# Performance work log

Measured on AMD Instinct MI355X. Metric: run time of the kernel, lower is better.

The kernel has to match this reference:

```python
import jax, jax.numpy as jnp
import numpy as np

N_AUTHORS = 50000
N_PAPERS = 100000
N_NODES = N_AUTHORS + N_PAPERS
N_EDGES = 1200000
EMB_DIM = 64
NUM_LAYERS = 3


def setup_inputs() -> dict:
    key = jax.random.key(0)
    k1, k2, k3, k4, k5 = jax.random.split(key, 5)
    author_embedding = jax.random.normal(k1, (N_AUTHORS, EMB_DIM), dtype=jnp.float32)
    paper_embedding = jax.random.normal(k2, (N_PAPERS, EMB_DIM), dtype=jnp.float32)
    adj_rows = jax.random.randint(k3, (N_EDGES,), 0, N_NODES, dtype=jnp.int32)
    adj_cols = jax.random.randint(k4, (N_EDGES,), 0, N_NODES, dtype=jnp.int32)
    # symmetric-normalized adjacency values are small positive floats
    adj_vals = jax.random.uniform(k5, (N_EDGES,), dtype=jnp.float32) * 0.1
    return {
        "author_embedding": author_embedding,
        "paper_embedding": paper_embedding,
        "adj_rows": adj_rows,
        "adj_cols": adj_cols,
        "adj_vals": adj_vals,
    }


def _spmm(adj_rows, adj_cols, adj_vals, x):
    # sparse [N,N] @ dense [N,d] via gather + segment_sum
    msgs = adj_vals[:, None] * x[adj_cols]  # [E, d]
    return jax.ops.segment_sum(msgs, adj_rows, num_segments=N_NODES)


def reference(author_embedding, paper_embedding, adj_rows, adj_cols, adj_vals):
    ego = jnp.concatenate([author_embedding, paper_embedding], axis=0)  # [N, d]
    acc = ego
    x = ego
    for _ in range(NUM_LAYERS):
        x = _spmm(adj_rows, adj_cols, adj_vals, x)
        acc = acc + x
    out = acc / jnp.float32(NUM_LAYERS + 1)  # mean over layer outputs
    out_author = out[:N_AUTHORS]
    out_paper = out[N_AUTHORS:]
    return ego, out_author, out_paper
```

## Files before the change

### kernel.cpp

```cpp
#include <hip/hip_runtime.h>

#define N_AUTHORS 50000
#define N_PAPERS  100000
#define N_NODES   150000
#define N_EDGES   1200000
#define EMB       64

#define BSHIFT 10
#define K_B    ((N_NODES + 1023) >> 10)
#define CHUNK  4096
#define NBLK_A ((N_EDGES + CHUNK - 1) / CHUNK)
#define NSC    (K_B * NBLK_A)
#define NBS1   ((NSC + 1023) / 1024)

__device__ __forceinline__ float bf2f(ushort u) {
    return __uint_as_float(((unsigned)u) << 16);
}
__device__ __forceinline__ ushort f2bf(float f) {
    unsigned u = __float_as_uint(f);
    return (ushort)((u + 0x7fffu + ((u >> 16) & 1u)) >> 16);
}

__global__ void lgcn_init(const float* __restrict__ a,
                          const float* __restrict__ p,
                          float* __restrict__ ego_out,
                          ushort* __restrict__ x0) {
    size_t i = (size_t)blockIdx.x * blockDim.x + threadIdx.x;
    const size_t n4  = (size_t)N_NODES  * EMB / 4;
    const size_t au4 = (size_t)N_AUTHORS * EMB / 4;
    if (i >= n4) return;
    float4 v = (i < au4) ? ((const float4*)a)[i] : ((const float4*)p)[i - au4];
    ((float4*)ego_out)[i] = v;
    ushort4 b;
    b.x = f2bf(v.x); b.y = f2bf(v.y); b.z = f2bf(v.z); b.w = f2bf(v.w);
    ((ushort4*)x0)[i] = b;
}

__global__ void lgcn_a0_hist(const int* __restrict__ rows,
                             unsigned* __restrict__ counts) {
    __shared__ unsigned h[K_B];
    int t = threadIdx.x;
    for (int i = t; i < K_B; i += blockDim.x) h[i] = 0;
    __syncthreads();
    int base = blockIdx.x * CHUNK;
    int end  = base + CHUNK; if (end > N_EDGES) end = N_EDGES;
    for (int e = base + t; e < end; e += blockDim.x)
        atomicAdd(&h[rows[e] >> BSHIFT], 1u);
    __syncthreads();
    for (int i = t; i < K_B; i += blockDim.x)
        counts[(size_t)i * NBLK_A + blockIdx.x] = h[i];
}

__global__ void lgcn_scan_l1(const unsigned* __restrict__ counts,
                             unsigned* __restrict__ scanned,
                             unsigned* __restrict__ btot) {
    __shared__ unsigned s[1024];
    int t = threadIdx.x;
    int i = blockIdx.x * 1024 + t;
    unsigned v = (i < NSC) ? counts[i] : 0u;
    s[t] = v;
    __syncthreads();
    for (int d = 1; d < 1024; d <<= 1) {
        unsigned u = (t >= d) ? s[t - d] : 0u;
        __syncthreads();
        s[t] += u;
        __syncthreads();
    }
    if (i < NSC) scanned[i] = s[t] - v;
    if (t == 1023) btot[blockIdx.x] = s[1023];
}

__global__ void lgcn_scan_l2(const unsigned* __restrict__ btot,
                             unsigned* __restrict__ btot_ex) {
    __shared__ unsigned s[64];
    int t = threadIdx.x;
    unsigned v = (t < NBS1) ? btot[t] : 0u;
    s[t] = v;
    __syncthreads();
    for (int d = 1; d < 64; d <<= 1) {
        unsigned u = (t >= d) ? s[t - d] : 0u;
        __syncthreads();
        s[t] += u;
        __syncthreads();
    }
    btot_ex[t] = s[t] - v;
}

__device__ __forceinline__ unsigned scan_at(const unsigned* scanned,
                                            const unsigned* btot_ex, unsigned idx) {
    return scanned[idx] + btot_ex[idx >> 10];
}

__global__ void lgcn_a1_bin(const int* __restrict__ rows,
                            const int* __restrict__ cols,
                            const float* __restrict__ vals,
                            const unsigned* __restrict__ scanned,
                            const unsigned* __restrict__ btot_ex,
                            float2* __restrict__ stage) {
    __shared__ unsigned cur[K_B];
    int t = threadIdx.x;
    for (int i = t; i < K_B; i += blockDim.x)
        cur[i] = scan_at(scanned, btot_ex, (unsigned)i * NBLK_A + blockIdx.x);
    __syncthreads();
    int base = blockIdx.x * CHUNK;
    int end  = base + CHUNK; if (end > N_EDGES) end = N_EDGES;
    for (int e = base + t; e < end; e += blockDim.x) {
        int r = rows[e];
        unsigned pos = atomicAdd(&cur[r >> BSHIFT], 1u);
        unsigned packed = ((unsigned)(r & 1023) << 18) | (unsigned)cols[e];
        stage[pos] = make_float2(__uint_as_float(packed), vals[e]);
    }
}

__global__ void lgcn_place(const unsigned* __restrict__ scanned,
                           const unsigned* __restrict__ btot_ex,
                           const float2* __restrict__ stage,
                           float2* __restrict__ se,
                           unsigned* __restrict__ row_start) {
    __shared__ unsigned cur[1 << BSHIFT];
    __shared__ unsigned tsum[256];
    int b  = blockIdx.x;
    int rb = b << BSHIFT;
    int nrows = N_NODES - rb; if (nrows > (1 << BSHIFT)) nrows = 1 << BSHIFT;
    int t = threadIdx.x;

    unsigned base  = scan_at(scanned, btot_ex, (unsigned)b * NBLK_A);
    unsigned span1 = (b + 1 < K_B)
                   ? scan_at(scanned, btot_ex, (unsigned)(b + 1) * NBLK_A)
                   : N_EDGES;

    for (int i = t; i < (1 << BSHIFT); i += 256) cur[i] = 0;
    __syncthreads();
    for (unsigned p = base + t; p < span1; p += 256)
        atomicAdd(&cur[__float_as_uint(stage[p].x) >> 18], 1u);
    __syncthreads();

    unsigned c[4], s = 0;
#pragma unroll
    for (int k = 0; k < 4; ++k) { c[k] = cur[t * 4 + k]; s += c[k]; }
    tsum[t] = s;
    __syncthreads();
    for (int d = 1; d < 256; d <<= 1) {
        unsigned u = (t >= d) ? tsum[t - d] : 0u;
        __syncthreads();
        tsum[t] += u;
        __syncthreads();
    }
    unsigned run = base + (tsum[t] - s);
    __syncthreads();
#pragma unroll
    for (int k = 0; k < 4; ++k) {
        int i = t * 4 + k;
        cur[i] = run;
        if (i < nrows) row_start[rb + i] = run;
        run += c[k];
    }
    if (b == K_B - 1 && t == 0) row_start[N_NODES] = N_EDGES;
    __syncthreads();

    for (unsigned p = base + t; p < span1; p += 256) {
        float2 v = stage[p];
        unsigned u = __float_as_uint(v.x);
        unsigned pos = atomicAdd(&cur[u >> 18], 1u);
        se[pos] = make_float2(__int_as_float((int)(u & 0x3FFFFu)), v.y);
    }
}

template <int FINAL>
__global__ void lgcn_spmm(const unsigned* __restrict__ rs,
                          const float2* __restrict__ se,
                          const ushort* __restrict__ x,
                          ushort* __restrict__ y,
                          const float* __restrict__ ego,
                          const ushort* __restrict__ y1,
                          const ushort* __restrict__ y2,
                          float* __restrict__ out) {
    int w    = blockIdx.x * (blockDim.x >> 6) + (threadIdx.x >> 6);
    int lane = threadIdx.x & 63;
    if (w >= N_NODES) return;
    unsigned j   = rs[w];
    unsigned end = rs[w + 1];
    const int g  = lane >> 3;
    const int d8 = (lane & 7) << 3;
    float a0=0.f,a1=0.f,a2=0.f,a3=0.f,a4=0.f,a5=0.f,a6=0.f,a7=0.f;

#define BATCH(JBASE)                                                          \
    {                                                                         \
        unsigned idx = (JBASE) + g;                                           \
        float2 e;                                                             \
        if (idx < end) e = se[idx];                                           \
        else { e.x = __int_as_float(0); e.y = 0.f; }                          \
        const uint4 xv = *(const uint4*)(x + ((size_t)__float_as_int(e.x) << 6) + d8); \
        a0 += e.y * __uint_as_float(xv.x << 16);                              \
        a1 += e.y * __uint_as_float(xv.x & 0xffff0000u);                      \
        a2 += e.y * __uint_as_float(xv.y << 16);                              \
        a3 += e.y * __uint_as_float(xv.y & 0xffff0000u);                      \
        a4 += e.y * __uint_as_float(xv.z << 16);                              \
        a5 += e.y * __uint_as_float(xv.z & 0xffff0000u);                      \
        a6 += e.y * __uint_as_float(xv.w << 16);                              \
        a7 += e.y * __uint_as_float(xv.w & 0xffff0000u);                      \
    }

    if (end - j > 8) {
        BATCH(j) BATCH(j + 8)
        j += 16;
    } else {
        BATCH(j)
        j += 8;
    }
    while (j < end) { BATCH(j) j += 8; }
#undef BATCH

    a0 += __shfl_xor(a0, 8, 64); a0 += __shfl_xor(a0, 16, 64); a0 += __shfl_xor(a0, 32, 64);
    a1 += __shfl_xor(a1, 8, 64); a1 += __shfl_xor(a1, 16, 64); a1 += __shfl_xor(a1, 32, 64);
    a2 += __shfl_xor(a2, 8, 64); a2 += __shfl_xor(a2, 16, 64); a2 += __shfl_xor(a2, 32, 64);
    a3 += __shfl_xor(a3, 8, 64); a3 += __shfl_xor(a3, 16, 64); a3 += __shfl_xor(a3, 32, 64);
    a4 += __shfl_xor(a4, 8, 64); a4 += __shfl_xor(a4, 16, 64); a4 += __shfl_xor(a4, 32, 64);
    a5 += __shfl_xor(a5, 8, 64); a5 += __shfl_xor(a5, 16, 64); a5 += __shfl_xor(a5, 32, 64);
    a6 += __shfl_xor(a6, 8, 64); a6 += __shfl_xor(a6, 16, 64); a6 += __shfl_xor(a6, 32, 64);
    a7 += __shfl_xor(a7, 8, 64); a7 += __shfl_xor(a7, 16, 64); a7 += __shfl_xor(a7, 32, 64);

    if (g == 0) {
        size_t o = ((size_t)w << 6) + d8;
        if (FINAL) {
            float4 e0 = *(const float4*)(ego + o);
            float4 e1 = *(const float4*)(ego + o + 4);
            uint4  u1 = *(const uint4*)(y1 + o);
            uint4  u2 = *(const uint4*)(y2 + o);
            float4 r0, r1;
            r0.x = 0.25f * (e0.x + __uint_as_float(u1.x << 16)        + __uint_as_float(u2.x << 16)        + a0);
            r0.y = 0.25f * (e0.y + __uint_as_float(u1.x & 0xffff0000u)+ __uint_as_float(u2.x & 0xffff0000u)+ a1);
            r0.z = 0.25f * (e0.z + __uint_as_float(u1.y << 16)        + __uint_as_float(u2.y << 16)        + a2);
            r0.w = 0.25f * (e0.w + __uint_as_float(u1.y & 0xffff0000u)+ __uint_as_float(u2.y & 0xffff0000u)+ a3);
            r1.x = 0.25f * (e1.x + __uint_as_float(u1.z << 16)        + __uint_as_float(u2.z << 16)        + a4);
            r1.y = 0.25f * (e1.y + __uint_as_float(u1.z & 0xffff0000u)+ __uint_as_float(u2.z & 0xffff0000u)+ a5);
            r1.z = 0.25f * (e1.z + __uint_as_float(u1.w << 16)        + __uint_as_float(u2.w << 16)        + a6);
            r1.w = 0.25f * (e1.w + __uint_as_float(u1.w & 0xffff0000u)+ __uint_as_float(u2.w & 0xffff0000u)+ a7);
            *(float4*)(out + o)     = r0;
            *(float4*)(out + o + 4) = r1;
        } else {
            uint4 ov;
            ov.x = (unsigned)f2bf(a0) | ((unsigned)f2bf(a1) << 16);
            ov.y = (unsigned)f2bf(a2) | ((unsigned)f2bf(a3) << 16);
            ov.z = (unsigned)f2bf(a4) | ((unsigned)f2bf(a5) << 16);
            ov.w = (unsigned)f2bf(a6) | ((unsigned)f2bf(a7) << 16);
            *(uint4*)(y + o) = ov;
        }
    }
}

extern "C" void kernel_launch(void* const* d_in, const int* in_sizes, int n_in,
                              void* d_out, int out_size, void* d_ws, size_t ws_size,
                              hipStream_t stream) {
    const float* author = (const float*)d_in[0];
    const float* paper  = (const float*)d_in[1];
    const int*   rows   = (const int*)d_in[2];
    const int*   cols   = (const int*)d_in[3];
    const float* vals   = (const float*)d_in[4];

    float* ego_out = (float*)d_out;
    float* acc     = (float*)d_out + (size_t)N_NODES * EMB;

    char* w = (char*)d_ws;
    float2*   se        = (float2*)w;   w += (size_t)N_EDGES * sizeof(float2);
    float2*   stage     = (float2*)w;   w += (size_t)N_EDGES * sizeof(float2);
    ushort*   xbE       = (ushort*)w;   w += (size_t)N_NODES * EMB * sizeof(ushort);
    ushort*   xb1       = (ushort*)w;   w += (size_t)N_NODES * EMB * sizeof(ushort);
    ushort*   xb2       = (ushort*)w;   w += (size_t)N_NODES * EMB * sizeof(ushort);
    unsigned* row_start = (unsigned*)w; w += (size_t)(N_NODES + 1) * 4;
    unsigned* bcounts   = (unsigned*)w; w += (size_t)NSC * 4;
    unsigned* bscanned  = (unsigned*)w; w += (size_t)NSC * 4;
    unsigned* btot      = (unsigned*)w; w += 64 * 4;
    unsigned* btot_ex   = (unsigned*)w; w += 64 * 4;

    const int BLK = 256;
    const int g_vec  = (int)(((size_t)N_NODES * EMB / 4 + BLK - 1) / BLK);
    const int g_spmm = (N_NODES + 3) / 4;

    lgcn_init<<<g_vec, BLK, 0, stream>>>(author, paper, ego_out, xbE);

    lgcn_a0_hist<<<NBLK_A, BLK, 0, stream>>>(rows, bcounts);
    lgcn_scan_l1<<<NBS1, 1024, 0, stream>>>(bcounts, bscanned, btot);
    lgcn_scan_l2<<<1, 64, 0, stream>>>(btot, btot_ex);

    lgcn_a1_bin<<<NBLK_A, BLK, 0, stream>>>(rows, cols, vals, bscanned, btot_ex, stage);
    lgcn_place<<<K_B, BLK, 0, stream>>>(bscanned, btot_ex, stage, se, row_start);

    lgcn_spmm<0><<<g_spmm, BLK, 0, stream>>>(row_start, se, xbE, xb1, nullptr, nullptr, nullptr, nullptr);
    lgcn_spmm<0><<<g_spmm, BLK, 0, stream>>>(row_start, se, xb1, xb2, nullptr, nullptr, nullptr, nullptr);
    lgcn_spmm<1><<<g_spmm, BLK, 0, stream>>>(row_start, se, xb2, nullptr, ego_out, xb1, xb2, acc);
}
```

Measured before the change: 212.9 us.

## Process two rows per wavefront in SpMM and read bf16 ego in final layer

Each 64-lane wavefront now handles two adjacent CSR rows, issuing their first gather batches back to back so two independent loads are in flight, and halving the grid size. The final layer reads the ego term from the bf16 copy instead of fp32 output, cutting bytes read. The cost is more registers per thread, possibly lower occupancy, and ego precision dropping to bf16 in the final mean.

```diff
diff --git a/kernel.cpp b/kernel.cpp
--- a/kernel.cpp
+++ b/kernel.cpp
@@ -171,45 +171,46 @@
                           const float2* __restrict__ se,
                           const ushort* __restrict__ x,
                           ushort* __restrict__ y,
-                          const float* __restrict__ ego,
+                          const ushort* __restrict__ egob,
                           const ushort* __restrict__ y1,
                           const ushort* __restrict__ y2,
                           float* __restrict__ out) {
     int w    = blockIdx.x * (blockDim.x >> 6) + (threadIdx.x >> 6);
     int lane = threadIdx.x & 63;
-    if (w >= N_NODES) return;
-    unsigned j   = rs[w];
-    unsigned end = rs[w + 1];
+    int r0   = w << 1;
+    if (r0 >= N_NODES) return;
+    unsigned jA   = rs[r0];
+    unsigned endA = rs[r0 + 1];
+    unsigned jB   = endA;
+    unsigned endB = rs[r0 + 2];
     const int g  = lane >> 3;
     const int d8 = (lane & 7) << 3;
     float a0=0.f,a1=0.f,a2=0.f,a3=0.f,a4=0.f,a5=0.f,a6=0.f,a7=0.f;
-
-#define BATCH(JBASE)                                                          \
+    float b0=0.f,b1=0.f,b2=0.f,b3=0.f,b4=0.f,b5=0.f,b6=0.f,b7=0.f;
+
+#define BATCH8(JB, END, P)                                                    \
     {                                                                         \
-        unsigned idx = (JBASE) + g;                                           \
+        unsigned idx = (JB) + g;                                              \
         float2 e;                                                             \
-        if (idx < end) e = se[idx];                                           \
+        if (idx < (END)) e = se[idx];                                         \
         else { e.x = __int_as_float(0); e.y = 0.f; }                          \
         const uint4 xv = *(const uint4*)(x + ((size_t)__float_as_int(e.x) << 6) + d8); \
-        a0 += e.y * __uint_as_float(xv.x << 16);                              \
-        a1 += e.y * __uint_as_float(xv.x & 0xffff0000u);                      \
-        a2 += e.y * __uint_as_float(xv.y << 16);                              \
-        a3 += e.y * __uint_as_float(xv.y & 0xffff0000u);                      \
-        a4 += e.y * __uint_as_float(xv.z << 16);                              \
-        a5 += e.y * __uint_as_float(xv.z & 0xffff0000u);                      \
-        a6 += e.y * __uint_as_float(xv.w << 16);                              \
-        a7 += e.y * __uint_as_float(xv.w & 0xffff0000u);                      \
-    }
-
-    if (end - j > 8) {
-        BATCH(j) BATCH(j + 8)
-        j += 16;
-    } else {
-        BATCH(j)
-        j += 8;
-    }
-    while (j < end) { BATCH(j) j += 8; }
-#undef BATCH
+        P##0 += e.y * __uint_as_float(xv.x << 16);                            \
+        P##1 += e.y * __uint_as_float(xv.x & 0xffff0000u);                    \
+        P##2 += e.y * __uint_as_float(xv.y << 16);                            \
+        P##3 += e.y * __uint_as_float(xv.y & 0xffff0000u);                    \
+        P##4 += e.y * __uint_as_float(xv.z << 16);                            \
+        P##5 += e.y * __uint_as_float(xv.z & 0xffff0000u);                    \
+        P##6 += e.y * __uint_as_float(xv.w << 16);                            \
+        P##7 += e.y * __uint_as_float(xv.w & 0xffff0000u);                    \
+    }
+
+    BATCH8(jA, endA, a)
+    BATCH8(jB, endB, b)
+    jA += 8; jB += 8;
+    while (jA < endA) { BATCH8(jA, endA, a) jA += 8; }
+    while (jB < endB) { BATCH8(jB, endB, b) jB += 8; }
+#undef BATCH8
 
     a0 += __shfl_xor(a0, 8, 64); a0 += __shfl_xor(a0, 16, 64); a0 += __shfl_xor(a0, 32, 64);
     a1 += __shfl_xor(a1, 8, 64); a1 += __shfl_xor(a1, 16, 64); a1 += __shfl_xor(a1, 32, 64);
@@ -219,32 +220,59 @@
     a5 += __shfl_xor(a5, 8, 64); a5 += __shfl_xor(a5, 16, 64); a5 += __shfl_xor(a5, 32, 64);
     a6 += __shfl_xor(a6, 8, 64); a6 += __shfl_xor(a6, 16, 64); a6 += __shfl_xor(a6, 32, 64);
     a7 += __shfl_xor(a7, 8, 64); a7 += __shfl_xor(a7, 16, 64); a7 += __shfl_xor(a7, 32, 64);
+    b0 += __shfl_xor(b0, 8, 64); b0 += __shfl_xor(b0, 16, 64); b0 += __shfl_xor(b0, 32, 64);
+    b1 += __shfl_xor(b1, 8, 64); b1 += __shfl_xor(b1, 16, 64); b1 += __shfl_xor(b1, 32, 64);
+    b2 += __shfl_xor(b2, 8, 64); b2 += __shfl_xor(b2, 16, 64); b2 += __shfl_xor(b2, 32, 64);
+    b3 += __shfl_xor(b3, 8, 64); b3 += __shfl_xor(b3, 16, 64); b3 += __shfl_xor(b3, 32, 64);
+    b4 += __shfl_xor(b4, 8, 64); b4 += __shfl_xor(b4, 16, 64); b4 += __shfl_xor(b4, 32, 64);
+    b5 += __shfl_xor(b5, 8, 64); b5 += __shfl_xor(b5, 16, 64); b5 += __shfl_xor(b5, 32, 64);
+    b6 += __shfl_xor(b6, 8, 64); b6 += __shfl_xor(b6, 16, 64); b6 += __shfl_xor(b6, 32, 64);
+    b7 += __shfl_xor(b7, 8, 64); b7 += __shfl_xor(b7, 16, 64); b7 += __shfl_xor(b7, 32, 64);
 
     if (g == 0) {
-        size_t o = ((size_t)w << 6) + d8;
+        size_t oA = ((size_t)r0 << 6) + d8;
+        size_t oB = oA + EMB;
         if (FINAL) {
-            float4 e0 = *(const float4*)(ego + o);
-            float4 e1 = *(const float4*)(ego + o + 4);
-            uint4  u1 = *(const uint4*)(y1 + o);
-            uint4  u2 = *(const uint4*)(y2 + o);
-            float4 r0, r1;
-            r0.x = 0.25f * (e0.x + __uint_as_float(u1.x << 16)        + __uint_as_float(u2.x << 16)        + a0);
-            r0.y = 0.25f * (e0.y + __uint_as_float(u1.x & 0xffff0000u)+ __uint_as_float(u2.x & 0xffff0000u)+ a1);
-            r0.z = 0.25f * (e0.z + __uint_as_float(u1.y << 16)        + __uint_as_float(u2.y << 16)        + a2);
-            r0.w = 0.25f * (e0.w + __uint_as_float(u1.y & 0xffff0000u)+ __uint_as_float(u2.y & 0xffff0000u)+ a3);
-            r1.x = 0.25f * (e1.x + __uint_as_float(u1.z << 16)        + __uint_as_float(u2.z << 16)        + a4);
-            r1.y = 0.25f * (e1.y + __uint_as_float(u1.z & 0xffff0000u)+ __uint_as_float(u2.z & 0xffff0000u)+ a5);
-            r1.z = 0.25f * (e1.z + __uint_as_float(u1.w << 16)        + __uint_as_float(u2.w << 16)        + a6);
-            r1.w = 0.25f * (e1.w + __uint_as_float(u1.w & 0xffff0000u)+ __uint_as_float(u2.w & 0xffff0000u)+ a7);
-            *(float4*)(out + o)     = r0;
-            *(float4*)(out + o + 4) = r1;
+            uint4 ue, u1, u2;
+            float4 r0v, r1v;
+            ue = *(const uint4*)(egob + oA);
+            u1 = *(const uint4*)(y1 + oA);
+            u2 = *(const uint4*)(y2 + oA);
+            r0v.x = 0.25f * (__uint_as_float(ue.x << 16)         + __uint_as_float(u1.x << 16)         + __uint_as_float(u2.x << 16)         + a0);
+            r0v.y = 0.25f * (__uint_as_float(ue.x & 0xffff0000u) + __uint_as_float(u1.x & 0xffff0000u) + __uint_as_float(u2.x & 0xffff0000u) + a1);
+            r0v.z = 0.25f * (__uint_as_float(ue.y << 16)         + __uint_as_float(u1.y << 16)         + __uint_as_float(u2.y << 16)         + a2);
+            r0v.w = 0.25f * (__uint_as_float(ue.y & 0xffff0000u) + __uint_as_float(u1.y & 0xffff0000u) + __uint_as_float(u2.y & 0xffff0000u) + a3);
+            r1v.x = 0.25f * (__uint_as_float(ue.z << 16)         + __uint_as_float(u1.z << 16)         + __uint_as_float(u2.z << 16)         + a4);
+            r1v.y = 0.25f * (__uint_as_float(ue.z & 0xffff0000u) + __uint_as_float(u1.z & 0xffff0000u) + __uint_as_float(u2.z & 0xffff0000u) + a5);
+            r1v.z = 0.25f * (__uint_as_float(ue.w << 16)         + __uint_as_float(u1.w << 16)         + __uint_as_float(u2.w << 16)         + a6);
+            r1v.w = 0.25f * (__uint_as_float(ue.w & 0xffff0000u) + __uint_as_float(u1.w & 0xffff0000u) + __uint_as_float(u2.w & 0xffff0000u) + a7);
+            *(float4*)(out + oA)     = r0v;
+            *(float4*)(out + oA + 4) = r1v;
+            ue = *(const uint4*)(egob + oB);
+            u1 = *(const uint4*)(y1 + oB);
+            u2 = *(const uint4*)(y2 + oB);
+            r0v.x = 0.25f * (__uint_as_float(ue.x << 16)         + __uint_as_float(u1.x << 16)         + __uint_as_float(u2.x << 16)         + b0);
+            r0v.y = 0.25f * (__uint_as_float(ue.x & 0xffff0000u) + __uint_as_float(u1.x & 0xffff0000u) + __uint_as_float(u2.x & 0xffff0000u) + b1);
+            r0v.z = 0.25f * (__uint_as_float(ue.y << 16)         + __uint_as_float(u1.y << 16)         + __uint_as_float(u2.y << 16)         + b2);
+            r0v.w = 0.25f * (__uint_as_float(ue.y & 0xffff0000u) + __uint_as_float(u1.y & 0xffff0000u) + __uint_as_float(u2.y & 0xffff0000u) + b3);
+            r1v.x = 0.25f * (__uint_as_float(ue.z << 16)         + __uint_as_float(u1.z << 16)         + __uint_as_float(u2.z << 16)         + b4);
+            r1v.y = 0.25f * (__uint_as_float(ue.z & 0xffff0000u) + __uint_as_float(u1.z & 0xffff0000u) + __uint_as_float(u2.z & 0xffff0000u) + b5);
+            r1v.z = 0.25f * (__uint_as_float(ue.w << 16)         + __uint_as_float(u1.w << 16)         + __uint_as_float(u2.w << 16)         + b6);
+            r1v.w = 0.25f * (__uint_as_float(ue.w & 0xffff0000u) + __uint_as_float(u1.w & 0xffff0000u) + __uint_as_float(u2.w & 0xffff0000u) + b7);
+            *(float4*)(out + oB)     = r0v;
+            *(float4*)(out + oB + 4) = r1v;
         } else {
             uint4 ov;
             ov.x = (unsigned)f2bf(a0) | ((unsigned)f2bf(a1) << 16);
             ov.y = (unsigned)f2bf(a2) | ((unsigned)f2bf(a3) << 16);
             ov.z = (unsigned)f2bf(a4) | ((unsigned)f2bf(a5) << 16);
             ov.w = (unsigned)f2bf(a6) | ((unsigned)f2bf(a7) << 16);
-            *(uint4*)(y + o) = ov;
+            *(uint4*)(y + oA) = ov;
+            ov.x = (unsigned)f2bf(b0) | ((unsigned)f2bf(b1) << 16);
+            ov.y = (unsigned)f2bf(b2) | ((unsigned)f2bf(b3) << 16);
+            ov.z = (unsigned)f2bf(b4) | ((unsigned)f2bf(b5) << 16);
+            ov.w = (unsigned)f2bf(b6) | ((unsigned)f2bf(b7) << 16);
+            *(uint4*)(y + oB) = ov;
         }
     }
 }
@@ -275,7 +303,7 @@
 
     const int BLK = 256;
     const int g_vec  = (int)(((size_t)N_NODES * EMB / 4 + BLK - 1) / BLK);
-    const int g_spmm = (N_NODES + 3) / 4;
+    const int g_spmm = ((N_NODES / 2) + 3) / 4;
 
     lgcn_init<<<g_vec, BLK, 0, stream>>>(author, paper, ego_out, xbE);
 
@@ -288,5 +316,5 @@
 
     lgcn_spmm<0><<<g_spmm, BLK, 0, stream>>>(row_start, se, xbE, xb1, nullptr, nullptr, nullptr, nullptr);
     lgcn_spmm<0><<<g_spmm, BLK, 0, stream>>>(row_start, se, xb1, xb2, nullptr, nullptr, nullptr, nullptr);
-    lgcn_spmm<1><<<g_spmm, BLK, 0, stream>>>(row_start, se, xb2, nullptr, ego_out, xb1, xb2, acc);
-}
+    lgcn_spmm<1><<<g_spmm, BLK, 0, stream>>>(row_start, se, xb2, nullptr, xbE, xb1, xb2, acc);
+}
```

Result: faster. 207.7 us (-2.5%).

## Process four rows per wavefront in SpMM and read bf16 ego in final layer

Applied to the files above, without the earlier changes.

The SpMM kernel now assigns four consecutive rows to each wavefront. It issues the first 8-edge gather batch for all four rows back to back to raise memory-level parallelism, then finishes any remaining edges row by row. The grid shrinks by a factor of four to match. The final layer also reads the bf16 copy of ego instead of the fp32 one, which halves that read but adds bf16 rounding to the ego term of the output. The cost is more accumulator registers per thread and serialized tail loops when one row's degree is much higher than the others in its group.

```diff
diff --git a/kernel.cpp b/kernel.cpp
--- a/kernel.cpp
+++ b/kernel.cpp
@@ -20,6 +20,8 @@
     unsigned u = __float_as_uint(f);
     return (ushort)((u + 0x7fffu + ((u >> 16) & 1u)) >> 16);
 }
+#define bfLO(u) __uint_as_float((u) << 16)
+#define bfHI(u) __uint_as_float((u) & 0xffff0000u)
 
 __global__ void lgcn_init(const float* __restrict__ a,
                           const float* __restrict__ p,
@@ -171,80 +173,89 @@
                           const float2* __restrict__ se,
                           const ushort* __restrict__ x,
                           ushort* __restrict__ y,
-                          const float* __restrict__ ego,
+                          const ushort* __restrict__ egob,
                           const ushort* __restrict__ y1,
                           const ushort* __restrict__ y2,
                           float* __restrict__ out) {
     int w    = blockIdx.x * (blockDim.x >> 6) + (threadIdx.x >> 6);
     int lane = threadIdx.x & 63;
-    if (w >= N_NODES) return;
-    unsigned j   = rs[w];
-    unsigned end = rs[w + 1];
+    int r0   = w << 2;
+    if (r0 >= N_NODES) return;
+    unsigned s0 = rs[r0];
+    unsigned s1 = rs[r0 + 1];
+    unsigned s2 = rs[r0 + 2];
+    unsigned s3 = rs[r0 + 3];
+    unsigned s4 = rs[r0 + 4];
     const int g  = lane >> 3;
     const int d8 = (lane & 7) << 3;
-    float a0=0.f,a1=0.f,a2=0.f,a3=0.f,a4=0.f,a5=0.f,a6=0.f,a7=0.f;
-
-#define BATCH(JBASE)                                                          \
+    float acc[4][8];
+#pragma unroll
+    for (int r = 0; r < 4; ++r)
+#pragma unroll
+        for (int k = 0; k < 8; ++k) acc[r][k] = 0.f;
+
+#define BATCH8(JB, END, R)                                                    \
     {                                                                         \
-        unsigned idx = (JBASE) + g;                                           \
+        unsigned idx = (JB) + g;                                              \
         float2 e;                                                             \
-        if (idx < end) e = se[idx];                                           \
+        if (idx < (END)) e = se[idx];                                         \
         else { e.x = __int_as_float(0); e.y = 0.f; }                          \
         const uint4 xv = *(const uint4*)(x + ((size_t)__float_as_int(e.x) << 6) + d8); \
-        a0 += e.y * __uint_as_float(xv.x << 16);                              \
-        a1 += e.y * __uint_as_float(xv.x & 0xffff0000u);                      \
-        a2 += e.y * __uint_as_float(xv.y << 16);                              \
-        a3 += e.y * __uint_as_float(xv.y & 0xffff0000u);                      \
-        a4 += e.y * __uint_as_float(xv.z << 16);                              \
-        a5 += e.y * __uint_as_float(xv.z & 0xffff0000u);                      \
-        a6 += e.y * __uint_as_float(xv.w << 16);                              \
-        a7 += e.y * __uint_as_float(xv.w & 0xffff0000u);                      \
-    }
-
-    if (end - j > 8) {
-        BATCH(j) BATCH(j + 8)
-        j += 16;
-    } else {
-        BATCH(j)
-        j += 8;
-    }
-    while (j < end) { BATCH(j) j += 8; }
-#undef BATCH
-
-    a0 += __shfl_xor(a0, 8, 64); a0 += __shfl_xor(a0, 16, 64); a0 += __shfl_xor(a0, 32, 64);
-    a1 += __shfl_xor(a1, 8, 64); a1 += __shfl_xor(a1, 16, 64); a1 += __shfl_xor(a1, 32, 64);
-    a2 += __shfl_xor(a2, 8, 64); a2 += __shfl_xor(a2, 16, 64); a2 += __shfl_xor(a2, 32, 64);
-    a3 += __shfl_xor(a3, 8, 64); a3 += __shfl_xor(a3, 16, 64); a3 += __shfl_xor(a3, 32, 64);
-    a4 += __shfl_xor(a4, 8, 64); a4 += __shfl_xor(a4, 16, 64); a4 += __shfl_xor(a4, 32, 64);
-    a5 += __shfl_xor(a5, 8, 64); a5 += __shfl_xor(a5, 16, 64); a5 += __shfl_xor(a5, 32, 64);
-    a6 += __shfl_xor(a6, 8, 64); a6 += __shfl_xor(a6, 16, 64); a6 += __shfl_xor(a6, 32, 64);
-    a7 += __shfl_xor(a7, 8, 64); a7 += __shfl_xor(a7, 16, 64); a7 += __shfl_xor(a7, 32, 64);
+        acc[R][0] += e.y * bfLO(xv.x); acc[R][1] += e.y * bfHI(xv.x);         \
+        acc[R][2] += e.y * bfLO(xv.y); acc[R][3] += e.y * bfHI(xv.y);         \
+        acc[R][4] += e.y * bfLO(xv.z); acc[R][5] += e.y * bfHI(xv.z);         \
+        acc[R][6] += e.y * bfLO(xv.w); acc[R][7] += e.y * bfHI(xv.w);         \
+    }
+
+    BATCH8(s0, s1, 0)
+    BATCH8(s1, s2, 1)
+    BATCH8(s2, s3, 2)
+    BATCH8(s3, s4, 3)
+    unsigned j0 = s0 + 8, j1 = s1 + 8, j2 = s2 + 8, j3 = s3 + 8;
+    while (j0 < s1) { BATCH8(j0, s1, 0) j0 += 8; }
+    while (j1 < s2) { BATCH8(j1, s2, 1) j1 += 8; }
+    while (j2 < s3) { BATCH8(j2, s3, 2) j2 += 8; }
+    while (j3 < s4) { BATCH8(j3, s4, 3) j3 += 8; }
+#undef BATCH8
+
+#pragma unroll
+    for (int r = 0; r < 4; ++r)
+#pragma unroll
+        for (int k = 0; k < 8; ++k) {
+            float v = acc[r][k];
+            v += __shfl_xor(v, 8, 64);
+            v += __shfl_xor(v, 16, 64);
+            v += __shfl_xor(v, 32, 64);
+            acc[r][k] = v;
+        }
 
     if (g == 0) {
-        size_t o = ((size_t)w << 6) + d8;
-        if (FINAL) {
-            float4 e0 = *(const float4*)(ego + o);
-            float4 e1 = *(const float4*)(ego + o + 4);
-            uint4  u1 = *(const uint4*)(y1 + o);
-            uint4  u2 = *(const uint4*)(y2 + o);
-            float4 r0, r1;
-            r0.x = 0.25f * (e0.x + __uint_as_float(u1.x << 16)        + __uint_as_float(u2.x << 16)        + a0);
-            r0.y = 0.25f * (e0.y + __uint_as_float(u1.x & 0xffff0000u)+ __uint_as_float(u2.x & 0xffff0000u)+ a1);
-            r0.z = 0.25f * (e0.z + __uint_as_float(u1.y << 16)        + __uint_as_float(u2.y << 16)        + a2);
-            r0.w = 0.25f * (e0.w + __uint_as_float(u1.y & 0xffff0000u)+ __uint_as_float(u2.y & 0xffff0000u)+ a3);
-            r1.x = 0.25f * (e1.x + __uint_as_float(u1.z << 16)        + __uint_as_float(u2.z << 16)        + a4);
-            r1.y = 0.25f * (e1.y + __uint_as_float(u1.z & 0xffff0000u)+ __uint_as_float(u2.z & 0xffff0000u)+ a5);
-            r1.z = 0.25f * (e1.z + __uint_as_float(u1.w << 16)        + __uint_as_float(u2.w << 16)        + a6);
-            r1.w = 0.25f * (e1.w + __uint_as_float(u1.w & 0xffff0000u)+ __uint_as_float(u2.w & 0xffff0000u)+ a7);
-            *(float4*)(out + o)     = r0;
-            *(float4*)(out + o + 4) = r1;
-        } else {
-            uint4 ov;
-            ov.x = (unsigned)f2bf(a0) | ((unsigned)f2bf(a1) << 16);
-            ov.y = (unsigned)f2bf(a2) | ((unsigned)f2bf(a3) << 16);
-            ov.z = (unsigned)f2bf(a4) | ((unsigned)f2bf(a5) << 16);
-            ov.w = (unsigned)f2bf(a6) | ((unsigned)f2bf(a7) << 16);
-            *(uint4*)(y + o) = ov;
+#pragma unroll
+        for (int r = 0; r < 4; ++r) {
+            size_t o = ((size_t)(r0 + r) << 6) + d8;
+            if (FINAL) {
+                uint4 ue = *(const uint4*)(egob + o);
+                uint4 u1 = *(const uint4*)(y1 + o);
+                uint4 u2 = *(const uint4*)(y2 + o);
+                float4 lo, hi;
+                lo.x = 0.25f * (bfLO(ue.x) + bfLO(u1.x) + bfLO(u2.x) + acc[r][0]);
+                lo.y = 0.25f * (bfHI(ue.x) + bfHI(u1.x) + bfHI(u2.x) + acc[r][1]);
+                lo.z = 0.25f * (bfLO(ue.y) + bfLO(u1.y) + bfLO(u2.y) + acc[r][2]);
+                lo.w = 0.25f * (bfHI(ue.y) + bfHI(u1.y) + bfHI(u2.y) + acc[r][3]);
+                hi.x = 0.25f * (bfLO(ue.z) + bfLO(u1.z) + bfLO(u2.z) + acc[r][4]);
+                hi.y = 0.25f * (bfHI(ue.z) + bfHI(u1.z) + bfHI(u2.z) + acc[r][5]);
+                hi.z = 0.25f * (bfLO(ue.w) + bfLO(u1.w) + bfLO(u2.w) + acc[r][6]);
+                hi.w = 0.25f * (bfHI(ue.w) + bfHI(u1.w) + bfHI(u2.w) + acc[r][7]);
+                *(float4*)(out + o)     = lo;
+                *(float4*)(out + o + 4) = hi;
+            } else {
+                uint4 ov;
+                ov.x = (unsigned)f2bf(acc[r][0]) | ((unsigned)f2bf(acc[r][1]) << 16);
+                ov.y = (unsigned)f2bf(acc[r][2]) | ((unsigned)f2bf(acc[r][3]) << 16);
+                ov.z = (unsigned)f2bf(acc[r][4]) | ((unsigned)f2bf(acc[r][5]) << 16);
+                ov.w = (unsigned)f2bf(acc[r][6]) | ((unsigned)f2bf(acc[r][7]) << 16);
+                *(uint4*)(y + o) = ov;
+            }
         }
     }
 }
@@ -275,7 +286,7 @@
 
     const int BLK = 256;
     const int g_vec  = (int)(((size_t)N_NODES * EMB / 4 + BLK - 1) / BLK);
-    const int g_spmm = (N_NODES + 3) / 4;
+    const int g_spmm = ((N_NODES / 4) + 3) / 4;
 
     lgcn_init<<<g_vec, BLK, 0, stream>>>(author, paper, ego_out, xbE);
 
@@ -288,5 +299,5 @@
 
     lgcn_spmm<0><<<g_spmm, BLK, 0, stream>>>(row_start, se, xbE, xb1, nullptr, nullptr, nullptr, nullptr);
     lgcn_spmm<0><<<g_spmm, BLK, 0, stream>>>(row_start, se, xb1, xb2, nullptr, nullptr, nullptr, nullptr);
-    lgcn_spmm<1><<<g_spmm, BLK, 0, stream>>>(row_start, se, xb2, nullptr, ego_out, xb1, xb2, acc);
-}
+    lgcn_spmm<1><<<g_spmm, BLK, 0, stream>>>(row_start, se, xb2, nullptr, xbE, xb1, xb2, acc);
+}
```

New measurement: 227.4 us. 6.8% more time.
